# Kernel optimization log

Measured on AMD Instinct MI355X. Metric: run time of the kernel, lower is better.

Reference implementation:

```python
import jax, jax.numpy as jnp
import numpy as np

# data_shape = (w, h, d, t); x viewed as torch (N, 1, D=w, H=h, W=d)
W_, H_, D_, T_ = 128, 128, 64, 100
INP = W_ * H_ * D_
K = 1


def _lin(n):
    # align_corners=False normalized coords (PyTorch affine_grid default)
    return (2.0 * jnp.arange(n, dtype=jnp.float32) + 1.0) / n - 1.0


def affine_grid(theta, Dm, Hm, Wm):
    # theta: (N, 3, 4) -> grid: (N, D, H, W, 3) with grid[...,0]=x(W), 1=y(H), 2=z(D)
    xs, ys, zs = _lin(Wm), _lin(Hm), _lin(Dm)
    base = jnp.stack([
        jnp.broadcast_to(xs[None, None, :], (Dm, Hm, Wm)),
        jnp.broadcast_to(ys[None, :, None], (Dm, Hm, Wm)),
        jnp.broadcast_to(zs[:, None, None], (Dm, Hm, Wm)),
        jnp.ones((Dm, Hm, Wm), jnp.float32),
    ], axis=-1)  # (D,H,W,4)
    return jnp.einsum('dhwb,nab->ndhwa', base, theta)


def grid_sample_3d(vol, grid):
    # vol: (N,D,H,W); grid: (N,D,H,W,3); trilinear, zeros padding, align_corners=False
    N, D, H, Wd = vol.shape
    ix = ((grid[..., 0] + 1.0) * Wd - 1.0) * 0.5
    iy = ((grid[..., 1] + 1.0) * H - 1.0) * 0.5
    iz = ((grid[..., 2] + 1.0) * D - 1.0) * 0.5
    x0 = jnp.floor(ix); y0 = jnp.floor(iy); z0 = jnp.floor(iz)
    tx, ty, tz = ix - x0, iy - y0, iz - z0
    x0i, y0i, z0i = x0.astype(jnp.int32), y0.astype(jnp.int32), z0.astype(jnp.int32)
    b = jnp.arange(N)[:, None, None, None]
    out = jnp.zeros_like(ix)
    for dz in (0, 1):
        for dy in (0, 1):
            for dx in (0, 1):
                xc, yc, zc = x0i + dx, y0i + dy, z0i + dz
                w = ((tx if dx else 1.0 - tx) * (ty if dy else 1.0 - ty)
                     * (tz if dz else 1.0 - tz))
                valid = ((xc >= 0) & (xc < Wd) & (yc >= 0) & (yc < H)
                         & (zc >= 0) & (zc < D))
                v = vol[b,
                        jnp.clip(zc, 0, D - 1),
                        jnp.clip(yc, 0, H - 1),
                        jnp.clip(xc, 0, Wd - 1)]
                out = out + jnp.where(valid, w * v, 0.0)
    return out


def setup_inputs() -> dict:
    key = jax.random.key(0)
    k1, k2, k3, k4 = jax.random.split(key, 4)
    x = jax.random.normal(k1, (8, INP), dtype=jnp.float32)
    r_index = jax.random.randint(k2, (8,), 0, T_)
    ident = jnp.array([[1., 0., 0., 0.], [0., 1., 0., 0.], [0., 0., 1., 0.]],
                      dtype=jnp.float32)
    theta = (jnp.tile(ident[None], (T_, 1, 1))
             + 0.01 * jax.random.normal(k3, (T_, 3, 4), dtype=jnp.float32))
    ln_weight = jax.random.normal(k4, (K, INP), dtype=jnp.float32) / np.sqrt(INP)
    return {"x": x, "r_index": r_index, "theta": theta, "ln_weight": ln_weight}


def reference(x, r_index, theta, ln_weight):
    n = x.shape[0]
    th = theta[r_index]                      # (n,3,4)
    vol = x.reshape(n, W_, H_, D_)           # torch (n,1,D=w,H=h,W=d), channel squeezed
    grid = affine_grid(th, W_, H_, D_)       # (n,w,h,d,3)
    x_reg = grid_sample_3d(vol, grid).reshape(n, INP)
    L = (x_reg @ ln_weight.T) @ ln_weight    # rank-k bottleneck: ln(x) @ ln.weight
    return x_reg, L
```

## Files before the change

### kernel.cpp

```cpp
#include <hip/hip_runtime.h>

#define INP (128*128*64)
#define NB 8
#define NBLK2 2048

typedef __attribute__((ext_vector_type(4))) float f32x4;
typedef __attribute__((ext_vector_type(2))) float f32x2;
typedef int v4i __attribute__((ext_vector_type(4)));

#if __has_builtin(__builtin_amdgcn_make_buffer_rsrc) && __has_builtin(__builtin_amdgcn_raw_buffer_load_b32)
#define RSRC_T __amdgpu_buffer_rsrc_t
__device__ __forceinline__ RSRC_T make_rsrc(const float* p) {
    return __builtin_amdgcn_make_buffer_rsrc((void*)p, (short)0, INP * 4, 0x00020000);
}
__device__ __forceinline__ float bload(RSRC_T r, int boff) {
    return __builtin_bit_cast(float, __builtin_amdgcn_raw_buffer_load_b32(r, boff, 0, 0));
}
#else
#define RSRC_T v4i
__device__ __forceinline__ RSRC_T make_rsrc(const float* p) {
    union { const float* p; unsigned u[2]; } pun; pun.p = p;
    RSRC_T r;
    r.x = (int)pun.u[0]; r.y = (int)pun.u[1]; r.z = INP * 4; r.w = 0x00020000;
    return r;
}
__device__ __forceinline__ float bload(RSRC_T r, int boff) {
    return __builtin_amdgcn_raw_buffer_load_f32(r, boff, 0, 0);
}
#endif

#if __has_builtin(__builtin_amdgcn_raw_buffer_load_b64)
__device__ __forceinline__ f32x2 bload2(RSRC_T r, int boff) {
    return __builtin_bit_cast(f32x2, __builtin_amdgcn_raw_buffer_load_b64(r, boff, 0, 0));
}
#else
__device__ __forceinline__ f32x2 bload2(RSRC_T r, int boff) {
    f32x2 v; v.x = bload(r, boff); v.y = bload(r, boff + 4); return v;
}
#endif

__device__ __forceinline__ float wave_reduce(float v) {
    #pragma unroll
    for (int off = 32; off > 0; off >>= 1) v += __shfl_down(v, off, 64);
    return v;
}

__device__ __forceinline__ float sample1(RSRC_T r, float ix, float iy, float iz) {
    const float fx = floorf(ix), fy = floorf(iy), fz = floorf(iz);
    const int x0 = (int)fx, y0 = (int)fy, z0 = (int)fz;
    const int x1 = x0 + 1,  y1 = y0 + 1,  z1 = z0 + 1;

    float wx1 = ix - fx, wx0 = 1.f - wx1;
    float wy1 = iy - fy, wy0 = 1.f - wy1;
    float wz1 = iz - fz, wz0 = 1.f - wz1;
    wx0 = ((unsigned)x0 < 64u)  ? wx0 : 0.f;
    wx1 = ((unsigned)x1 < 64u)  ? wx1 : 0.f;
    wy0 = ((unsigned)y0 < 128u) ? wy0 : 0.f;
    wy1 = ((unsigned)y1 < 128u) ? wy1 : 0.f;
    wz0 = ((unsigned)z0 < 128u) ? wz0 : 0.f;
    wz1 = ((unsigned)z1 < 128u) ? wz1 : 0.f;

    const int yc0 = min(max(y0, 0), 127), yc1 = min(max(y1, 0), 127);
    const int zc0 = min(max(z0, 0), 127), zc1 = min(max(z1, 0), 127);
    const int xpb = min(max(x0, 0), 62) << 2;
    const int yb0 = (yc0 << 8) + xpb, yb1 = (yc1 << 8) + xpb;
    const int zb0 = zc0 << 15,        zb1 = zc1 << 15;

    const f32x2 p00 = bload2(r, zb0 + yb0);
    const f32x2 p01 = bload2(r, zb0 + yb1);
    const f32x2 p10 = bload2(r, zb1 + yb0);
    const f32x2 p11 = bload2(r, zb1 + yb1);

    const bool hi = (x0 >= 63);
    const bool lo = (x0 < 0);
    const float v000 = hi ? p00.y : p00.x, v001 = lo ? p00.x : p00.y;
    const float v010 = hi ? p01.y : p01.x, v011 = lo ? p01.x : p01.y;
    const float v100 = hi ? p10.y : p10.x, v101 = lo ? p10.x : p10.y;
    const float v110 = hi ? p11.y : p11.x, v111 = lo ? p11.x : p11.y;

    const float bx00 = fmaf(wx1, v001, wx0 * v000);
    const float bx01 = fmaf(wx1, v011, wx0 * v010);
    const float bx10 = fmaf(wx1, v101, wx0 * v100);
    const float bx11 = fmaf(wx1, v111, wx0 * v110);
    const float by0  = fmaf(wy1, bx01, wy0 * bx00);
    const float by1  = fmaf(wy1, bx11, wy0 * bx10);
    return fmaf(wz1, by1, wz0 * by0);
}

__global__ __launch_bounds__(256) void k_sample(
    const float* __restrict__ x, const int* __restrict__ r_index,
    const float* __restrict__ theta, const float* __restrict__ lnw,
    float* __restrict__ x_reg, float* __restrict__ partial)
{
    const int b  = blockIdx.y;
    const int i2 = blockIdx.x * 256 + threadIdx.x;
    const int w0 = (i2 & 31) << 1;
    const int h  = (i2 >> 5) & 127;
    const int d  = i2 >> 12;

    const f32x2 w2 = ((const f32x2*)lnw)[i2];

    const float xs = fmaf((float)w0, 1.f/32.f, 1.f/64.f  - 1.f);
    const float ys = fmaf((float)h,  1.f/64.f, 1.f/128.f - 1.f);
    const float zs = fmaf((float)d,  1.f/64.f, 1.f/128.f - 1.f);

    const float* __restrict__ t = theta + r_index[b] * 12;
    const float gx = fmaf(t[0], xs, fmaf(t[1], ys, fmaf(t[2],  zs, t[3])));
    const float gy = fmaf(t[4], xs, fmaf(t[5], ys, fmaf(t[6],  zs, t[7])));
    const float gz = fmaf(t[8], xs, fmaf(t[9], ys, fmaf(t[10], zs, t[11])));
    const float ix0 = fmaf(gx, 32.f, 31.5f);
    const float iy0 = fmaf(gy, 64.f, 63.5f);
    const float iz0 = fmaf(gz, 64.f, 63.5f);

    const RSRC_T r = make_rsrc(x + (size_t)b * INP);
    const float o0 = sample1(r, ix0, iy0, iz0);
    const float o1 = sample1(r, ix0 + t[0], iy0 + 2.f*t[4], iz0 + 2.f*t[8]);

    f32x2 o; o.x = o0; o.y = o1;
    __builtin_nontemporal_store(o, (f32x2*)(x_reg + (size_t)b * INP) + i2);

    float acc = fmaf(o1, w2.y, o0 * w2.x);
    acc = wave_reduce(acc);
    __shared__ float sm[4];
    const int lane = threadIdx.x & 63;
    const int wv   = threadIdx.x >> 6;
    if (lane == 0) sm[wv] = acc;
    __syncthreads();
    if (threadIdx.x == 0)
        partial[b * NBLK2 + blockIdx.x] = sm[0] + sm[1] + sm[2] + sm[3];
}

__global__ __launch_bounds__(256) void k_reduce(
    const float* __restrict__ partial, float* __restrict__ s)
{
    const int b = blockIdx.x;
    float v = 0.f;
    for (int t = threadIdx.x; t < NBLK2; t += 256) v += partial[b * NBLK2 + t];
    __shared__ float sm[4];
    v = wave_reduce(v);
    if ((threadIdx.x & 63) == 0) sm[threadIdx.x >> 6] = v;
    __syncthreads();
    if (threadIdx.x == 0) s[b] = sm[0] + sm[1] + sm[2] + sm[3];
}

__global__ __launch_bounds__(256) void k_outer(
    const float* __restrict__ lnw, const float* __restrict__ s,
    float* __restrict__ L)
{
    const int i = blockIdx.x * 256 + threadIdx.x;
    const f32x4 w4 = ((const f32x4*)lnw)[i];
    #pragma unroll
    for (int b = 0; b < NB; ++b) {
        const float sb = s[b];
        f32x4 o = sb * w4;
        __builtin_nontemporal_store(o, (f32x4*)(L + (size_t)b * INP) + i);
    }
}

extern "C" void kernel_launch(void* const* d_in, const int* in_sizes, int n_in,
                              void* d_out, int out_size, void* d_ws, size_t ws_size,
                              hipStream_t stream) {
    const float* x       = (const float*)d_in[0];
    const int*   r_index = (const int*)d_in[1];
    const float* theta   = (const float*)d_in[2];
    const float* lnw     = (const float*)d_in[3];

    float* x_reg = (float*)d_out;
    float* L     = (float*)d_out + (size_t)NB * INP;

    float* partial = (float*)d_ws;
    float* s       = partial + NB * NBLK2;

    dim3 grid1(NBLK2, NB);
    k_sample<<<grid1, 256, 0, stream>>>(x, r_index, theta, lnw, x_reg, partial);
    k_reduce<<<NB, 256, 0, stream>>>(partial, s);
    k_outer<<<INP / 4 / 256, 256, 0, stream>>>(lnw, s, L);
}
```

Measured before the change: 39.53 us.

## Fuse partial-sum reduction into outer-product kernel and batch sampler gathers

Removes the separate k_reduce launch. Each k_outer block now recomputes the per-batch sum from the 2048 partials and then writes its slice of L for one batch, on a 2D grid over blocks and batches. The sampler is split into an index/weight prep phase and a blend phase, so all eight 8-byte gathers for both samples are issued before any arithmetic. The x-boundary selects are folded into the two x weights. This costs some redundant partial reads in every k_outer block and more registers held live in the sampler.

```diff
diff --git a/kernel.cpp b/kernel.cpp
--- a/kernel.cpp
+++ b/kernel.cpp
@@ -45,46 +45,50 @@
     return v;
 }
 
-__device__ __forceinline__ float sample1(RSRC_T r, float ix, float iy, float iz) {
+struct Prep {
+    int o[4];
+    float wa, wb, wy0, wy1, wz0, wz1;
+};
+
+__device__ __forceinline__ Prep prep_s(float ix, float iy, float iz) {
     const float fx = floorf(ix), fy = floorf(iy), fz = floorf(iz);
     const int x0 = (int)fx, y0 = (int)fy, z0 = (int)fz;
     const int x1 = x0 + 1,  y1 = y0 + 1,  z1 = z0 + 1;
 
-    float wx1 = ix - fx, wx0 = 1.f - wx1;
-    float wy1 = iy - fy, wy0 = 1.f - wy1;
-    float wz1 = iz - fz, wz0 = 1.f - wz1;
-    wx0 = ((unsigned)x0 < 64u)  ? wx0 : 0.f;
-    wx1 = ((unsigned)x1 < 64u)  ? wx1 : 0.f;
-    wy0 = ((unsigned)y0 < 128u) ? wy0 : 0.f;
-    wy1 = ((unsigned)y1 < 128u) ? wy1 : 0.f;
-    wz0 = ((unsigned)z0 < 128u) ? wz0 : 0.f;
-    wz1 = ((unsigned)z1 < 128u) ? wz1 : 0.f;
+    const float wx1 = ix - fx, wx0 = 1.f - wx1;
+    Prep p;
+    p.wy1 = iy - fy; p.wy0 = 1.f - p.wy1;
+    p.wz1 = iz - fz; p.wz0 = 1.f - p.wz1;
+    p.wy0 = ((unsigned)y0 < 128u) ? p.wy0 : 0.f;
+    p.wy1 = ((unsigned)y1 < 128u) ? p.wy1 : 0.f;
+    p.wz0 = ((unsigned)z0 < 128u) ? p.wz0 : 0.f;
+    p.wz1 = ((unsigned)z1 < 128u) ? p.wz1 : 0.f;
+
+    const float wx0z = ((unsigned)x0 < 64u) ? wx0 : 0.f;
+    const float wx1z = ((unsigned)x1 < 64u) ? wx1 : 0.f;
+    const bool hi = (x0 >= 63);
+    const bool lo = (x0 < 0);
+    p.wa = lo ? wx1z : (hi ? 0.f : wx0z);
+    p.wb = hi ? wx0z : (lo ? 0.f : wx1z);
 
     const int yc0 = min(max(y0, 0), 127), yc1 = min(max(y1, 0), 127);
     const int zc0 = min(max(z0, 0), 127), zc1 = min(max(z1, 0), 127);
     const int xpb = min(max(x0, 0), 62) << 2;
     const int yb0 = (yc0 << 8) + xpb, yb1 = (yc1 << 8) + xpb;
     const int zb0 = zc0 << 15,        zb1 = zc1 << 15;
+    p.o[0] = zb0 + yb0; p.o[1] = zb0 + yb1;
+    p.o[2] = zb1 + yb0; p.o[3] = zb1 + yb1;
+    return p;
+}
 
-    const f32x2 p00 = bload2(r, zb0 + yb0);
-    const f32x2 p01 = bload2(r, zb0 + yb1);
-    const f32x2 p10 = bload2(r, zb1 + yb0);
-    const f32x2 p11 = bload2(r, zb1 + yb1);
-
-    const bool hi = (x0 >= 63);
-    const bool lo = (x0 < 0);
-    const float v000 = hi ? p00.y : p00.x, v001 = lo ? p00.x : p00.y;
-    const float v010 = hi ? p01.y : p01.x, v011 = lo ? p01.x : p01.y;
-    const float v100 = hi ? p10.y : p10.x, v101 = lo ? p10.x : p10.y;
-    const float v110 = hi ? p11.y : p11.x, v111 = lo ? p11.x : p11.y;
-
-    const float bx00 = fmaf(wx1, v001, wx0 * v000);
-    const float bx01 = fmaf(wx1, v011, wx0 * v010);
-    const float bx10 = fmaf(wx1, v101, wx0 * v100);
-    const float bx11 = fmaf(wx1, v111, wx0 * v110);
-    const float by0  = fmaf(wy1, bx01, wy0 * bx00);
-    const float by1  = fmaf(wy1, bx11, wy0 * bx10);
-    return fmaf(wz1, by1, wz0 * by0);
+__device__ __forceinline__ float blend_s(const Prep& p, const f32x2 v[4]) {
+    const float bx00 = fmaf(p.wb, v[0].y, p.wa * v[0].x);
+    const float bx01 = fmaf(p.wb, v[1].y, p.wa * v[1].x);
+    const float bx10 = fmaf(p.wb, v[2].y, p.wa * v[2].x);
+    const float bx11 = fmaf(p.wb, v[3].y, p.wa * v[3].x);
+    const float by0  = fmaf(p.wy1, bx01, p.wy0 * bx00);
+    const float by1  = fmaf(p.wy1, bx11, p.wy0 * bx10);
+    return fmaf(p.wz1, by1, p.wz0 * by0);
 }
 
 __global__ __launch_bounds__(256) void k_sample(
@@ -113,8 +117,18 @@
     const float iz0 = fmaf(gz, 64.f, 63.5f);
 
     const RSRC_T r = make_rsrc(x + (size_t)b * INP);
-    const float o0 = sample1(r, ix0, iy0, iz0);
-    const float o1 = sample1(r, ix0 + t[0], iy0 + 2.f*t[4], iz0 + 2.f*t[8]);
+
+    const Prep p0 = prep_s(ix0, iy0, iz0);
+    const Prep p1 = prep_s(ix0 + t[0], iy0 + 2.f*t[4], iz0 + 2.f*t[8]);
+
+    f32x2 v0[4], v1[4];
+    #pragma unroll
+    for (int j = 0; j < 4; ++j) v0[j] = bload2(r, p0.o[j]);
+    #pragma unroll
+    for (int j = 0; j < 4; ++j) v1[j] = bload2(r, p1.o[j]);
+
+    const float o0 = blend_s(p0, v0);
+    const float o1 = blend_s(p1, v1);
 
     f32x2 o; o.x = o0; o.y = o1;
     __builtin_nontemporal_store(o, (f32x2*)(x_reg + (size_t)b * INP) + i2);
@@ -122,38 +136,39 @@
     float acc = fmaf(o1, w2.y, o0 * w2.x);
     acc = wave_reduce(acc);
     __shared__ float sm[4];
-    const int lane = threadIdx.x & 63;
-    const int wv   = threadIdx.x >> 6;
-    if (lane == 0) sm[wv] = acc;
+    if ((threadIdx.x & 63) == 0) sm[threadIdx.x >> 6] = acc;
     __syncthreads();
     if (threadIdx.x == 0)
         partial[b * NBLK2 + blockIdx.x] = sm[0] + sm[1] + sm[2] + sm[3];
 }
 
-__global__ __launch_bounds__(256) void k_reduce(
-    const float* __restrict__ partial, float* __restrict__ s)
-{
-    const int b = blockIdx.x;
-    float v = 0.f;
-    for (int t = threadIdx.x; t < NBLK2; t += 256) v += partial[b * NBLK2 + t];
-    __shared__ float sm[4];
-    v = wave_reduce(v);
-    if ((threadIdx.x & 63) == 0) sm[threadIdx.x >> 6] = v;
-    __syncthreads();
-    if (threadIdx.x == 0) s[b] = sm[0] + sm[1] + sm[2] + sm[3];
-}
-
 __global__ __launch_bounds__(256) void k_outer(
-    const float* __restrict__ lnw, const float* __restrict__ s,
+    const float* __restrict__ lnw, const float* __restrict__ partial,
     float* __restrict__ L)
 {
-    const int i = blockIdx.x * 256 + threadIdx.x;
-    const f32x4 w4 = ((const f32x4*)lnw)[i];
+    const int b   = blockIdx.y;
+    const int tid = threadIdx.x;
+
+    const f32x4* p4 = (const f32x4*)(partial + b * NBLK2);
+    const f32x4 a0 = p4[tid];
+    const f32x4 a1 = p4[tid + 256];
+    float v = (a0.x + a0.y) + (a0.z + a0.w) + (a1.x + a1.y) + (a1.z + a1.w);
+    v = wave_reduce(v);
+    __shared__ float sm[4];
+    __shared__ float smt;
+    if ((tid & 63) == 0) sm[tid >> 6] = v;
+    __syncthreads();
+    if (tid == 0) smt = (sm[0] + sm[1]) + (sm[2] + sm[3]);
+    __syncthreads();
+    const float sb = smt;
+
+    const int base = blockIdx.x * 2048 + tid;
+    const f32x4* w4p = (const f32x4*)lnw;
+    f32x4* L4 = (f32x4*)L + (size_t)b * (INP / 4);
     #pragma unroll
-    for (int b = 0; b < NB; ++b) {
-        const float sb = s[b];
-        f32x4 o = sb * w4;
-        __builtin_nontemporal_store(o, (f32x4*)(L + (size_t)b * INP) + i);
+    for (int k = 0; k < 8; ++k) {
+        const f32x4 w4 = w4p[base + k * 256];
+        __builtin_nontemporal_store(sb * w4, L4 + base + k * 256);
     }
 }
 
@@ -169,10 +184,9 @@
     float* L     = (float*)d_out + (size_t)NB * INP;
 
     float* partial = (float*)d_ws;
-    float* s       = partial + NB * NBLK2;
 
     dim3 grid1(NBLK2, NB);
     k_sample<<<grid1, 256, 0, stream>>>(x, r_index, theta, lnw, x_reg, partial);
-    k_reduce<<<NB, 256, 0, stream>>>(partial, s);
-    k_outer<<<INP / 4 / 256, 256, 0, stream>>>(lnw, s, L);
+    dim3 grid2(128, NB);
+    k_outer<<<grid2, 256, 0, stream>>>(lnw, partial, L);
 }
```

New measurement: 33.96 us. 1.16x faster.
